# Optimization experiments

Hardware: AMD Instinct MI355X
Metric: run time of the kernel (lower is better)

Reference implementation:

```python
import jax, jax.numpy as jnp
import numpy as np

N = 4096

def setup_inputs() -> dict:
    key = jax.random.key(0)
    kA, kB = jax.random.split(key)
    # A and B are upper-triangular inputs, as the module assumes
    A = jnp.triu(jax.random.normal(kA, (N, N), dtype=jnp.float32))
    B = jnp.triu(jax.random.normal(kB, (N, N), dtype=jnp.float32))
    return {"A": A, "B": B}

def reference(A, B):
    # C = triu(A @ B); product of upper-triangular matrices is upper-triangular,
    # the kernel additionally masks the lower triangle of the output.
    return jnp.triu(A @ B)
```

## Files before the change

kernel.cpp:

```cpp
#include <hip/hip_runtime.h>


#define N    4096
#define NB   32
#define BM   128
#define PK   64
#define NWG  512
#define NJOB 528
#define RS   72

typedef __attribute__((ext_vector_type(8))) __bf16 bf16x8;
typedef __attribute__((ext_vector_type(4))) float  floatx4;
typedef __attribute__((ext_vector_type(8))) unsigned short ushort8;

__device__ __forceinline__ unsigned short f32_to_bf16_rne(float f) {
    unsigned u = __builtin_bit_cast(unsigned, f);
    unsigned r = u + 0x7fffu + ((u >> 16) & 1u);
    return (unsigned short)(r >> 16);
}

__global__ __launch_bounds__(256)
void prep_kernel(const float* __restrict__ A, const float* __restrict__ B,
                 unsigned short* __restrict__ Ab, unsigned short* __restrict__ Bt,
                 float* __restrict__ C) {
    __shared__ float tile[64][65];
    const int bx = blockIdx.x, by = blockIdx.y;
    const int x0 = bx * 64, y0 = by * 64;
    const int xb = bx >> 1, yb = by >> 1;
    const int t  = threadIdx.x;
    const int tr = t >> 2, tc = (t & 3) * 16;

    if (xb >= yb) {
        const float* src = A + (size_t)(y0 + tr) * N + x0 + tc;
        const float4 v0 = ((const float4*)src)[0];
        const float4 v1 = ((const float4*)src)[1];
        const float4 v2 = ((const float4*)src)[2];
        const float4 v3 = ((const float4*)src)[3];
        ushort8 o0, o1;
        o0[0]=f32_to_bf16_rne(v0.x); o0[1]=f32_to_bf16_rne(v0.y);
        o0[2]=f32_to_bf16_rne(v0.z); o0[3]=f32_to_bf16_rne(v0.w);
        o0[4]=f32_to_bf16_rne(v1.x); o0[5]=f32_to_bf16_rne(v1.y);
        o0[6]=f32_to_bf16_rne(v1.z); o0[7]=f32_to_bf16_rne(v1.w);
        o1[0]=f32_to_bf16_rne(v2.x); o1[1]=f32_to_bf16_rne(v2.y);
        o1[2]=f32_to_bf16_rne(v2.z); o1[3]=f32_to_bf16_rne(v2.w);
        o1[4]=f32_to_bf16_rne(v3.x); o1[5]=f32_to_bf16_rne(v3.y);
        o1[6]=f32_to_bf16_rne(v3.z); o1[7]=f32_to_bf16_rne(v3.w);
        unsigned short* dst = Ab + (size_t)(y0 + tr) * N + x0 + tc;
        ((ushort8*)dst)[0] = o0;
        ((ushort8*)dst)[1] = o1;
    }
    if (xb <= yb) {
        const float* src = B + (size_t)(x0 + tr) * N + y0 + tc;
        const float4 v0 = ((const float4*)src)[0];
        const float4 v1 = ((const float4*)src)[1];
        const float4 v2 = ((const float4*)src)[2];
        const float4 v3 = ((const float4*)src)[3];
        float* d = &tile[tr][tc];
        d[0]=v0.x; d[1]=v0.y; d[2]=v0.z; d[3]=v0.w;
        d[4]=v1.x; d[5]=v1.y; d[6]=v1.z; d[7]=v1.w;
        d[8]=v2.x; d[9]=v2.y; d[10]=v2.z; d[11]=v2.w;
        d[12]=v3.x; d[13]=v3.y; d[14]=v3.z; d[15]=v3.w;
        __syncthreads();
        ushort8 o0, o1;
        #pragma unroll
        for (int i = 0; i < 8; ++i) o0[i] = f32_to_bf16_rne(tile[tc + i][tr]);
        #pragma unroll
        for (int i = 0; i < 8; ++i) o1[i] = f32_to_bf16_rne(tile[tc + 8 + i][tr]);
        unsigned short* dst = Bt + (size_t)(y0 + tr) * N + x0 + tc;
        ((ushort8*)dst)[0] = o0;
        ((ushort8*)dst)[1] = o1;
    }
    if (xb < yb) {
        float4 z = {0.f, 0.f, 0.f, 0.f};
        float* dst = C + (size_t)(y0 + tr) * N + x0 + tc;
        ((float4*)dst)[0] = z; ((float4*)dst)[1] = z;
        ((float4*)dst)[2] = z; ((float4*)dst)[3] = z;
    }
}

__global__ __launch_bounds__(256, 2)
void trimm_kernel(const unsigned short* __restrict__ Ab,
                  const unsigned short* __restrict__ Bt,
                  float* __restrict__ C) {
    __shared__ unsigned short sA[2][BM * RS];
    __shared__ unsigned short sB[2][BM * RS];

    const int tid  = threadIdx.x;
    const int w    = tid >> 6;
    const int lane = tid & 63;
    const int quad = lane >> 4;
    const int l15  = lane & 15;

    const int m0 = (w >> 1) * 64;
    const int n0 = (w & 1) * 64;

    const int srow8 = lane >> 3;
    const int sk    = (lane & 7) * 8;
    int lofs[4], rr[4];
    #pragma unroll
    for (int i = 0; i < 4; ++i) {
        rr[i]   = w * 32 + i * 8 + srow8;
        lofs[i] = rr[i] * RS + sk;
    }

    for (int p = 0;; ++p) {
        const int idx = p * NWG + ((p & 1) ? (NWG - 1 - (int)blockIdx.x)
                                           : (int)blockIdx.x);
        if (idx >= NJOB) break;

        int rem = idx, d = NB - 1;
        for (; d >= 0; --d) {
            const int cnt = NB - d;
            if (rem < cnt) break;
            rem -= cnt;
        }
        const int bi = rem, bj = bi + d;
        const int row0 = bi * BM;
        const int col0 = bj * BM;

        floatx4 acc[4][4] = {};

        const unsigned short* gA[4];
        const unsigned short* gB[4];
        #pragma unroll
        for (int i = 0; i < 4; ++i) {
            gA[i] = Ab + (size_t)(row0 + rr[i]) * N + bi * BM + sk;
            gB[i] = Bt + (size_t)(col0 + rr[i]) * N + bi * BM + sk;
        }

        const int np = (d + 1) * 2;

        ushort8 aR[4], bR[4];
        #pragma unroll
        for (int i = 0; i < 4; ++i) { aR[i] = *(const ushort8*)gA[i]; gA[i] += PK; }
        #pragma unroll
        for (int i = 0; i < 4; ++i) { bR[i] = *(const ushort8*)gB[i]; gB[i] += PK; }

        for (int ph = 0; ph < np - 1; ++ph) {
            const int buf = ph & 1;
            #pragma unroll
            for (int i = 0; i < 4; ++i) *(ushort8*)&sA[buf][lofs[i]] = aR[i];
            #pragma unroll
            for (int i = 0; i < 4; ++i) *(ushort8*)&sB[buf][lofs[i]] = bR[i];
            __syncthreads();
            #pragma unroll
            for (int i = 0; i < 4; ++i) { aR[i] = *(const ushort8*)gA[i]; gA[i] += PK; }
            #pragma unroll
            for (int i = 0; i < 4; ++i) { bR[i] = *(const ushort8*)gB[i]; gB[i] += PK; }
            #pragma unroll
            for (int h = 0; h < 2; ++h) {
                bf16x8 af[4], bfr[4];
                #pragma unroll
                for (int t = 0; t < 4; ++t) {
                    af[t]  = *(const bf16x8*)&sA[buf][(m0 + t * 16 + l15) * RS + h * 32 + quad * 8];
                    bfr[t] = *(const bf16x8*)&sB[buf][(n0 + t * 16 + l15) * RS + h * 32 + quad * 8];
                }
                #pragma unroll
                for (int tm = 0; tm < 4; ++tm)
                    #pragma unroll
                    for (int tn = 0; tn < 4; ++tn)
                        acc[tm][tn] = __builtin_amdgcn_mfma_f32_16x16x32_bf16(
                            af[tm], bfr[tn], acc[tm][tn], 0, 0, 0);
            }
        }
        {
            const int buf = (np - 1) & 1;
            #pragma unroll
            for (int i = 0; i < 4; ++i) *(ushort8*)&sA[buf][lofs[i]] = aR[i];
            #pragma unroll
            for (int i = 0; i < 4; ++i) *(ushort8*)&sB[buf][lofs[i]] = bR[i];
            __syncthreads();
            #pragma unroll
            for (int h = 0; h < 2; ++h) {
                bf16x8 af[4], bfr[4];
                #pragma unroll
                for (int t = 0; t < 4; ++t) {
                    af[t]  = *(const bf16x8*)&sA[buf][(m0 + t * 16 + l15) * RS + h * 32 + quad * 8];
                    bfr[t] = *(const bf16x8*)&sB[buf][(n0 + t * 16 + l15) * RS + h * 32 + quad * 8];
                }
                #pragma unroll
                for (int tm = 0; tm < 4; ++tm)
                    #pragma unroll
                    for (int tn = 0; tn < 4; ++tn)
                        acc[tm][tn] = __builtin_amdgcn_mfma_f32_16x16x32_bf16(
                            af[tm], bfr[tn], acc[tm][tn], 0, 0, 0);
            }
            __syncthreads();
        }

        #pragma unroll
        for (int tm = 0; tm < 4; ++tm) {
            const int grow_base = row0 + m0 + tm * 16 + quad * 4;
            #pragma unroll
            for (int tn = 0; tn < 4; ++tn) {
                const int gcol = col0 + n0 + tn * 16 + l15;
                #pragma unroll
                for (int r = 0; r < 4; ++r) {
                    const int grow = grow_base + r;
                    const float v = acc[tm][tn][r];
                    if (d != 0) {
                        C[(size_t)grow * N + gcol] = v;
                    } else {
                        C[(size_t)grow * N + gcol] = (gcol >= grow) ? v : 0.0f;
                    }
                }
            }
        }
    }
}

extern "C" void kernel_launch(void* const* d_in, const int* in_sizes, int n_in,
                              void* d_out, int out_size, void* d_ws, size_t ws_size,
                              hipStream_t stream) {
    const float* A = (const float*)d_in[0];
    const float* B = (const float*)d_in[1];
    float* C = (float*)d_out;

    unsigned short* Ab = (unsigned short*)d_ws;
    unsigned short* Bt = Ab + (size_t)N * N;

    prep_kernel<<<dim3(N / 64, N / 64), dim3(256), 0, stream>>>(A, B, Ab, Bt, C);
    trimm_kernel<<<dim3(NWG), dim3(256), 0, stream>>>(Ab, Bt, C);
}
```

Before: 231.7 us.

## Split long triangular tiles along K and balance with static greedy schedule

Replaces the round-robin tile assignment with a compile-time schedule that splits tiles with long K ranges into chunks of at most 24 phases, then assigns chunks to workgroups with a longest-first greedy load balancer. Split chunks accumulate into C with atomicAdd, and the prep kernel now pre-zeroes the far-diagonal output blocks that receive atomics. This aims to remove the load imbalance from triangular tiles of very different lengths, at the cost of atomic traffic and a nondeterministic summation order.

```diff
diff --git a/kernel.cpp b/kernel.cpp
--- a/kernel.cpp
+++ b/kernel.cpp
@@ -6,12 +6,78 @@
 #define BM   128
 #define PK   64
 #define NWG  512
-#define NJOB 528
 #define RS   72
+#define CH   24
+#define MAXF 832
+#define MAXL 64
 
 typedef __attribute__((ext_vector_type(8))) __bf16 bf16x8;
 typedef __attribute__((ext_vector_type(4))) float  floatx4;
 typedef __attribute__((ext_vector_type(8))) unsigned short ushort8;
+
+struct Sched {
+    unsigned short wgoff[NWG + 1];
+    unsigned int   chunks[MAXF];
+    int nf;
+};
+
+constexpr Sched make_sched() {
+    Sched s{};
+    unsigned int fr_sz[MAXF] = {};
+    unsigned int fr_pk[MAXF] = {};
+    int nf = 0;
+    for (int d = NB - 1; d >= 0; --d) {
+        const int npj  = 2 * (d + 1);
+        const int nc   = (npj + CH - 1) / CH;
+        const int base = npj / nc, rem = npj % nc;
+        for (int bi = 0; bi + d < NB; ++bi) {
+            const int bj = bi + d;
+            int p0 = 0;
+            for (int c = 0; c < nc; ++c) {
+                const int fnp = base + (c < rem ? 1 : 0);
+                fr_sz[nf] = (unsigned)fnp;
+                fr_pk[nf] = (unsigned)bi | ((unsigned)bj << 5) |
+                            ((unsigned)p0 << 10) | ((unsigned)fnp << 17) |
+                            ((nc > 1 ? 1u : 0u) << 24);
+                ++nf;
+                p0 += fnp;
+            }
+        }
+    }
+    int order[MAXF] = {};
+    int pos = 0;
+    for (int sz = CH; sz >= 1; --sz)
+        for (int i = 0; i < nf; ++i)
+            if ((int)fr_sz[i] == sz) order[pos++] = i;
+    int bcnt[MAXL] = {};
+    int blist[MAXL][NWG] = {};
+    for (int b = 0; b < NWG; ++b) blist[0][b] = NWG - 1 - b;
+    bcnt[0] = NWG;
+    int assign[MAXF] = {};
+    int minload = 0;
+    for (int k = 0; k < nf; ++k) {
+        const int f = order[k];
+        while (bcnt[minload] == 0) ++minload;
+        const int b  = blist[minload][--bcnt[minload]];
+        const int nl = minload + (int)fr_sz[f];
+        blist[nl][bcnt[nl]++] = b;
+        assign[f] = b;
+    }
+    int cnt[NWG] = {};
+    for (int f = 0; f < nf; ++f) cnt[assign[f]]++;
+    s.wgoff[0] = 0;
+    for (int b = 0; b < NWG; ++b)
+        s.wgoff[b + 1] = (unsigned short)(s.wgoff[b] + cnt[b]);
+    int fill[NWG] = {};
+    for (int f = 0; f < nf; ++f) {
+        const int b = assign[f];
+        s.chunks[s.wgoff[b] + fill[b]++] = fr_pk[f];
+    }
+    s.nf = nf;
+    return s;
+}
+
+__device__ constexpr Sched g_sched = make_sched();
 
 __device__ __forceinline__ unsigned short f32_to_bf16_rne(float f) {
     unsigned u = __builtin_bit_cast(unsigned, f);
@@ -70,7 +136,7 @@
         ((ushort8*)dst)[0] = o0;
         ((ushort8*)dst)[1] = o1;
     }
-    if (xb < yb) {
+    if (xb < yb || (xb - yb) >= 12) {
         float4 z = {0.f, 0.f, 0.f, 0.f};
         float* dst = C + (size_t)(y0 + tr) * N + x0 + tc;
         ((float4*)dst)[0] = z; ((float4*)dst)[1] = z;
@@ -103,20 +169,21 @@
         lofs[i] = rr[i] * RS + sk;
     }
 
-    for (int p = 0;; ++p) {
-        const int idx = p * NWG + ((p & 1) ? (NWG - 1 - (int)blockIdx.x)
-                                           : (int)blockIdx.x);
-        if (idx >= NJOB) break;
-
-        int rem = idx, d = NB - 1;
-        for (; d >= 0; --d) {
-            const int cnt = NB - d;
-            if (rem < cnt) break;
-            rem -= cnt;
-        }
-        const int bi = rem, bj = bi + d;
+    const int b  = (int)blockIdx.x;
+    const int j0 = g_sched.wgoff[b];
+    const int j1 = g_sched.wgoff[b + 1];
+
+    for (int j = j0; j < j1; ++j) {
+        const unsigned int ck = g_sched.chunks[j];
+        const int bi   = ck & 31;
+        const int bj   = (ck >> 5) & 31;
+        const int p0   = (ck >> 10) & 127;
+        const int cnp  = (ck >> 17) & 127;
+        const bool is_at = (ck >> 24) & 1u;
+
         const int row0 = bi * BM;
         const int col0 = bj * BM;
+        const int k0   = bi * BM + p0 * PK;
 
         floatx4 acc[4][4] = {};
 
@@ -124,11 +191,9 @@
         const unsigned short* gB[4];
         #pragma unroll
         for (int i = 0; i < 4; ++i) {
-            gA[i] = Ab + (size_t)(row0 + rr[i]) * N + bi * BM + sk;
-            gB[i] = Bt + (size_t)(col0 + rr[i]) * N + bi * BM + sk;
-        }
-
-        const int np = (d + 1) * 2;
+            gA[i] = Ab + (size_t)(row0 + rr[i]) * N + k0 + sk;
+            gB[i] = Bt + (size_t)(col0 + rr[i]) * N + k0 + sk;
+        }
 
         ushort8 aR[4], bR[4];
         #pragma unroll
@@ -136,7 +201,7 @@
         #pragma unroll
         for (int i = 0; i < 4; ++i) { bR[i] = *(const ushort8*)gB[i]; gB[i] += PK; }
 
-        for (int ph = 0; ph < np - 1; ++ph) {
+        for (int ph = 0; ph < cnp - 1; ++ph) {
             const int buf = ph & 1;
             #pragma unroll
             for (int i = 0; i < 4; ++i) *(ushort8*)&sA[buf][lofs[i]] = aR[i];
@@ -164,7 +229,7 @@
             }
         }
         {
-            const int buf = (np - 1) & 1;
+            const int buf = (cnp - 1) & 1;
             #pragma unroll
             for (int i = 0; i < 4; ++i) *(ushort8*)&sA[buf][lofs[i]] = aR[i];
             #pragma unroll
@@ -198,7 +263,9 @@
                 for (int r = 0; r < 4; ++r) {
                     const int grow = grow_base + r;
                     const float v = acc[tm][tn][r];
-                    if (d != 0) {
+                    if (is_at) {
+                        atomicAdd(&C[(size_t)grow * N + gcol], v);
+                    } else if (bi != bj) {
                         C[(size_t)grow * N + gcol] = v;
                     } else {
                         C[(size_t)grow * N + gcol] = (gcol >= grow) ? v : 0.0f;
```

Measured after the change: 219.9 us. 1.05x faster.
